# Kernel tuning notes

Measured on AMD Instinct MI355X. Metric: run time of the kernel, lower is better.

Reference implementation:

```python
import jax, jax.numpy as jnp
import numpy as np

B, T, D = 4, 2048, 1024
N_HEADS = 16
D_HEAD = D // N_HEADS


def setup_inputs() -> dict:
    key = jax.random.key(0)
    ks = jax.random.split(key, 5)
    s = 1.0 / np.sqrt(D)  # keep activations well-scaled
    return {
        "x": jax.random.normal(ks[0], (B, T, D), dtype=jnp.float32),
        "Wq": jax.random.normal(ks[1], (D, D), dtype=jnp.float32) * s,
        "Wk": jax.random.normal(ks[2], (D, D), dtype=jnp.float32) * s,
        "Wv": jax.random.normal(ks[3], (D, D), dtype=jnp.float32) * s,
        "Wo": jax.random.normal(ks[4], (D, D), dtype=jnp.float32) * s,
    }


def reference(x, Wq, Wk, Wv, Wo):
    Bx, Tx, C = x.shape
    # projections; nn.Linear(d,d,bias=False): y = x @ W^T
    def split_heads(y):
        return y.reshape(Bx, Tx, N_HEADS, D_HEAD).transpose(0, 2, 1, 3)  # [B,H,T,dh]
    q = split_heads(x @ Wq.T)
    k = split_heads(x @ Wk.T)
    v = split_heads(x @ Wv.T)
    scale = 1.0 / np.sqrt(D_HEAD)
    att = jnp.einsum("bhtd,bhsd->bhts", q, k) * scale  # [B,H,T,T]
    causal = jnp.tril(jnp.ones((Tx, Tx), dtype=bool))
    att = jnp.where(causal[None, None], att, -jnp.inf)
    att = jax.nn.softmax(att, axis=-1)
    y = jnp.einsum("bhts,bhsd->bhtd", att, v)  # [B,H,T,dh]
    y = y.transpose(0, 2, 1, 3).reshape(Bx, Tx, C)
    return y @ Wo.T
```

## Files before the change

### kernel.cpp

```cpp
#include <hip/hip_runtime.h>
#include <cstdint>
#include <cstddef>

typedef unsigned short u16;
typedef short bf16x8 __attribute__((ext_vector_type(8)));
typedef unsigned short u16x8 __attribute__((ext_vector_type(8)));
typedef float f32x4 __attribute__((ext_vector_type(4)));
typedef float f32x16 __attribute__((ext_vector_type(16)));
typedef unsigned u32x2 __attribute__((ext_vector_type(2)));

__device__ __forceinline__ u16 f2bf(float x) {
    union { float f; unsigned int u; } v; v.f = x;
    unsigned int u = v.u;
    unsigned int r = (u + 0x7fffu + ((u >> 16) & 1u)) >> 16;
    return (u16)r;
}

__device__ __forceinline__ unsigned cvtpk(float lo, float hi) {
    unsigned r;
    asm("v_cvt_pk_bf16_f32 %0, %1, %2" : "=v"(r) : "v"(lo), "v"(hi));
    return r;
}

__device__ __forceinline__ float exp2v(float x) {
    float y;
    asm("v_exp_f32 %0, %1" : "=v"(y) : "v"(x));
    return y;
}

__device__ __forceinline__ void load_lds16(const void* g, void* l) {
    __builtin_amdgcn_global_load_lds((const __attribute__((address_space(1))) void*)g,
                                     (__attribute__((address_space(3))) void*)l, 16, 0, 0);
}

__global__ void cast_f32_bf16(const float* __restrict__ in, u16* __restrict__ out, int n) {
    int i = (blockIdx.x * blockDim.x + threadIdx.x) * 4;
    int stride = gridDim.x * blockDim.x * 4;
    for (; i < n; i += stride) {
        float4 f = *reinterpret_cast<const float4*>(in + i);
        ushort4 o;
        o.x = f2bf(f.x); o.y = f2bf(f.y); o.z = f2bf(f.z); o.w = f2bf(f.w);
        *reinterpret_cast<ushort4*>(out + i) = o;
    }
}

__global__ void cast_w4(const float* __restrict__ w0, const float* __restrict__ w1,
                        const float* __restrict__ w2, const float* __restrict__ w3,
                        u16* __restrict__ out, int nw) {
    const int wsel = blockIdx.y;
    const float* in = (wsel == 0) ? w0 : (wsel == 1) ? w1 : (wsel == 2) ? w2 : w3;
    u16* o = out + (size_t)wsel * nw;
    int i = (blockIdx.x * blockDim.x + threadIdx.x) * 4;
    int stride = gridDim.x * blockDim.x * 4;
    for (; i < nw; i += stride) {
        float4 f = *reinterpret_cast<const float4*>(in + i);
        ushort4 v;
        v.x = f2bf(f.x); v.y = f2bf(f.y); v.z = f2bf(f.z); v.w = f2bf(f.w);
        *reinterpret_cast<ushort4*>(o + i) = v;
    }
}

template <int MODE>
__global__ __launch_bounds__(256) void gemm_bt(const u16* __restrict__ A,
                                               const u16* __restrict__ Bw,
                                               void* __restrict__ outp,
                                               u16* __restrict__ vtg,
                                               int M, int N, int K) {
    __shared__ u16 smem[16384];
    u16* As = smem;
    u16* Bs = smem + 4096;

    const int tid  = threadIdx.x;
    const int m0   = blockIdx.x * 128;
    const int n0   = blockIdx.y * 128;
    const int wid  = tid >> 6;
    const int lane = tid & 63;
    const int wr   = (wid >> 1) * 64;
    const int wc   = (wid & 1) * 64;
    const int fr   = lane & 15;
    const int ko   = (lane >> 4) * 8;
    const int rq   = (lane >> 4) * 4;

    f32x4 acc[4][4];
#pragma unroll
    for (int i = 0; i < 4; ++i)
#pragma unroll
        for (int j = 0; j < 4; ++j) acc[i][j] = f32x4{0.f, 0.f, 0.f, 0.f};

    const int lr4 = lane >> 2;
    const int ls  = lane & 3;

    for (int k0 = 0; k0 < K; k0 += 32) {
#pragma unroll
        for (int t = 0; t < 2; ++t) {
            const int qtr = wid * 2 + t;
            const int r   = qtr * 16 + lr4;
            load_lds16(&A[(size_t)(m0 + r) * K + k0 + ls * 8], &As[qtr * 512]);
            load_lds16(&Bw[(size_t)(n0 + r) * K + k0 + ls * 8], &Bs[qtr * 512]);
        }
        __syncthreads();

        bf16x8 af[4], bfr[4];
#pragma unroll
        for (int mf = 0; mf < 4; ++mf)
            af[mf] = *reinterpret_cast<const bf16x8*>(&As[(wr + mf * 16 + fr) * 32 + ko]);
#pragma unroll
        for (int nf = 0; nf < 4; ++nf)
            bfr[nf] = *reinterpret_cast<const bf16x8*>(&Bs[(wc + nf * 16 + fr) * 32 + ko]);
        __builtin_amdgcn_s_setprio(1);
#pragma unroll
        for (int mf = 0; mf < 4; ++mf)
#pragma unroll
            for (int nf = 0; nf < 4; ++nf)
                acc[mf][nf] = __builtin_amdgcn_mfma_f32_16x16x32_bf16(
                    af[mf], bfr[nf], acc[mf][nf], 0, 0, 0);
        __builtin_amdgcn_s_setprio(0);
        __syncthreads();
    }

    if constexpr (MODE == 0) {
        float* C = (float*)outp;
#pragma unroll
        for (int mf = 0; mf < 4; ++mf)
#pragma unroll
            for (int nf = 0; nf < 4; ++nf)
#pragma unroll
                for (int i = 0; i < 4; ++i)
                    C[(size_t)(m0 + wr + mf * 16 + rq + i) * N + n0 + wc + nf * 16 + fr] =
                        acc[mf][nf][i];
    } else {
        if (n0 < 2048) {
            const float osc = (n0 < 1024) ? 0.18033688011112042f : 1.0f;
            u16* qk = (u16*)outp;
#pragma unroll
            for (int mf = 0; mf < 4; ++mf)
#pragma unroll
                for (int nf = 0; nf < 4; ++nf)
#pragma unroll
                    for (int i = 0; i < 4; ++i)
                        qk[(size_t)(m0 + wr + mf * 16 + rq + i) * 2048 + n0 + wc + nf * 16 + fr] =
                            f2bf(acc[mf][nf][i] * osc);
        } else {
#pragma unroll
            for (int mf = 0; mf < 4; ++mf)
#pragma unroll
                for (int nf = 0; nf < 4; ++nf) {
                    const int nl  = wc + nf * 16 + fr;
                    const int ml0 = wr + mf * 16 + rq;
                    uint2 pk;
                    pk.x = cvtpk(acc[mf][nf][0], acc[mf][nf][1]);
                    pk.y = cvtpk(acc[mf][nf][2], acc[mf][nf][3]);
                    *reinterpret_cast<uint2*>(
                        &smem[nl * 128 + ((((ml0 * 2) ^ ((nl & 15) << 4))) >> 1)]) = pk;
                }
            __syncthreads();
            const int bb   = m0 >> 11;
            const int tloc = m0 & 2047;
#pragma unroll
            for (int p = 0; p < 8; ++p) {
                const int nl = (tid >> 4) + p * 16;
                const int sl = tid & 15;
                u16x8 v = *reinterpret_cast<const u16x8*>(
                    &smem[nl * 128 + ((((sl * 16) ^ ((nl & 15) << 4))) >> 1)]);
                *reinterpret_cast<u16x8*>(
                    &vtg[(size_t)(bb * 1024 + (n0 - 2048) + nl) * 2048 + tloc + sl * 8]) = v;
            }
        }
    }
}

__global__ __launch_bounds__(128) void attn_fwd(const u16* __restrict__ qk,
                                                const u16* __restrict__ vtg,
                                                u16* __restrict__ Y) {
    constexpr int T = 2048, DQK = 2048, DOUT = 1024;
    const int bh = blockIdx.x;
    const int jb = blockIdx.y;
    const int b  = bh >> 4, hd = bh & 15;
    const int tid = threadIdx.x, w = tid >> 6, lane = tid & 63;
    const int qloc = lane & 31, h2 = lane >> 5;

    __shared__ u16 Ks[2][4096];
    __shared__ u16 Vs[2][4096];

    const size_t rowb = (size_t)b * T;
    const int sr8 = lane >> 3, ss = lane & 7;
    const int sc = (ss ^ sr8) * 8;

#define BUILD_PA(sv, RB, dst) {                                               \
        unsigned wa  = cvtpk(sv[RB + 0], sv[RB + 1]);                         \
        unsigned wb  = cvtpk(sv[RB + 2], sv[RB + 3]);                         \
        unsigned wc2 = cvtpk(sv[RB + 4], sv[RB + 5]);                         \
        unsigned wd  = cvtpk(sv[RB + 6], sv[RB + 7]);                         \
        u32x2 r0 = __builtin_amdgcn_permlane32_swap(wa, wc2, false, false);   \
        u32x2 r1 = __builtin_amdgcn_permlane32_swap(wb, wd, false, false);    \
        dst.x = r0.x; dst.y = r1.x; dst.z = r0.y; dst.w = r1.y; }

#define PV_STEP(pa, KS, ROWBASE, oacc) {                                      \
        const int rr_ = (ROWBASE) + qloc;                                     \
        bf16x8 vf_ = *reinterpret_cast<const bf16x8*>(                        \
            &Vb[rr_ * 64 + (((2 * (KS) + h2) ^ (rr_ & 7)) * 8)]);             \
        oacc = __builtin_amdgcn_mfma_f32_32x32x16_bf16(                       \
            *reinterpret_cast<const bf16x8*>(&pa), vf_, oacc, 0, 0, 0); }

    for (int qi = 0; qi < 2; ++qi) {
        const int qt = (qi == 0) ? (31 - jb) : jb;
        const int q0 = qt * 64;
        const int wq = q0 + w * 32;
        const int NT = qt + 1;

        bf16x8 qf[4];
#pragma unroll
        for (int ks = 0; ks < 4; ++ks)
            qf[ks] = *reinterpret_cast<const bf16x8*>(
                &qk[(rowb + wq + qloc) * DQK + hd * 64 + ks * 16 + h2 * 8]);

        f32x16 o0, o1;
#pragma unroll
        for (int i = 0; i < 16; ++i) { o0[i] = 0.f; o1[i] = 0.f; }
        float lp = 0.f;

        const u16* kp[4];
        const u16* vp[4];
#pragma unroll
        for (int t = 0; t < 4; ++t) {
            const int r = (w * 4 + t) * 8 + sr8;
            kp[t] = qk + (rowb + r) * DQK + 1024 + hd * 64 + sc;
            vp[t] = vtg + ((size_t)bh * 64 + r) * T + sc;
        }

        __syncthreads();

#pragma unroll
        for (int t = 0; t < 4; ++t) {
            const int chunk = w * 4 + t;
            load_lds16(kp[t], &Ks[0][chunk * 512]);
            load_lds16(vp[t], &Vs[0][chunk * 512]);
        }
#pragma unroll
        for (int t = 0; t < 4; ++t) { kp[t] += 64 * DQK; vp[t] += 64; }

        for (int kt = 0; kt < NT; ++kt) {
            __syncthreads();

            if (kt + 1 < NT) {
                const int nb = (kt + 1) & 1;
#pragma unroll
                for (int t = 0; t < 4; ++t) {
                    const int chunk = w * 4 + t;
                    load_lds16(kp[t], &Ks[nb][chunk * 512]);
                    load_lds16(vp[t], &Vs[nb][chunk * 512]);
                }
#pragma unroll
                for (int t = 0; t < 4; ++t) { kp[t] += 64 * DQK; vp[t] += 64; }
            }

            const int k0 = kt * 64;
            if (k0 <= wq + 31) {
                const u16* Kb = Ks[kt & 1];
                const u16* Vb = Vs[kt & 1];
                const bool do1 = (k0 + 32 <= wq + 31);
                const bool dm  = (k0 + 63 > wq);

                f32x16 st0, st1;
#pragma unroll
                for (int i = 0; i < 16; ++i) { st0[i] = 0.f; st1[i] = 0.f; }

                __builtin_amdgcn_s_setprio(1);
#pragma unroll
                for (int ks = 0; ks < 4; ++ks) {
                    bf16x8 kf = *reinterpret_cast<const bf16x8*>(
                        &Kb[qloc * 64 + (((2 * ks + h2) ^ (qloc & 7)) * 8)]);
                    st0 = __builtin_amdgcn_mfma_f32_32x32x16_bf16(kf, qf[ks], st0, 0, 0, 0);
                }
                if (do1) {
#pragma unroll
                    for (int ks = 0; ks < 4; ++ks) {
                        const int r1 = 32 + qloc;
                        bf16x8 kf = *reinterpret_cast<const bf16x8*>(
                            &Kb[r1 * 64 + (((2 * ks + h2) ^ (r1 & 7)) * 8)]);
                        st1 = __builtin_amdgcn_mfma_f32_32x32x16_bf16(kf, qf[ks], st1, 0, 0, 0);
                    }
                }
                __builtin_amdgcn_s_setprio(0);

                const int qg = wq + qloc;
#pragma unroll
                for (int i = 0; i < 16; ++i) st0[i] = exp2v(st0[i]);
                if (do1) {
#pragma unroll
                    for (int i = 0; i < 16; ++i) st1[i] = exp2v(st1[i]);
                }
                if (dm) {
#pragma unroll
                    for (int r = 0; r < 16; ++r) {
                        const int crow = (r & 3) + 8 * (r >> 2) + 4 * h2;
                        if (k0 + crow > qg)      st0[r] = 0.f;
                        if (k0 + 32 + crow > qg) st1[r] = 0.f;
                    }
                }
                {
                    float l0 = 0.f, l1 = 0.f, l2 = 0.f, l3 = 0.f;
#pragma unroll
                    for (int i = 0; i < 4; ++i) {
                        l0 += st0[i]; l1 += st0[4 + i]; l2 += st0[8 + i]; l3 += st0[12 + i];
                    }
                    if (do1) {
#pragma unroll
                        for (int i = 0; i < 4; ++i) {
                            l0 += st1[i]; l1 += st1[4 + i]; l2 += st1[8 + i]; l3 += st1[12 + i];
                        }
                    }
                    lp += (l0 + l1) + (l2 + l3);
                }

                uint4 pa0, pa1, pa2, pa3;
                BUILD_PA(st0, 0, pa0);
                BUILD_PA(st0, 8, pa1);
                if (do1) {
                    BUILD_PA(st1, 0, pa2);
                    BUILD_PA(st1, 8, pa3);
                }

                __builtin_amdgcn_s_setprio(1);
                PV_STEP(pa0, 0, 0, o0);
                PV_STEP(pa1, 1, 0, o0);
                PV_STEP(pa0, 0, 32, o1);
                PV_STEP(pa1, 1, 32, o1);
                if (do1) {
                    PV_STEP(pa2, 2, 0, o0);
                    PV_STEP(pa3, 3, 0, o0);
                    PV_STEP(pa2, 2, 32, o1);
                    PV_STEP(pa3, 3, 32, o1);
                }
                __builtin_amdgcn_s_setprio(0);
            }
        }

        const float lf = lp + __shfl_xor(lp, 32);
        const float linv = 1.0f / lf;
#pragma unroll
        for (int r = 0; r < 16; ++r) {
            const int crow = (r & 3) + 8 * (r >> 2) + 4 * h2;
            const float rl = __shfl(linv, crow);
            const size_t yrow = rowb + wq + crow;
            Y[yrow * DOUT + hd * 64 + qloc]      = (u16)cvtpk(o0[r] * rl, 0.f);
            Y[yrow * DOUT + hd * 64 + 32 + qloc] = (u16)cvtpk(o1[r] * rl, 0.f);
        }
    }
#undef BUILD_PA
#undef PV_STEP
}

extern "C" void kernel_launch(void* const* d_in, const int* in_sizes, int n_in,
                              void* d_out, int out_size, void* d_ws, size_t ws_size,
                              hipStream_t stream) {
    const float* x  = (const float*)d_in[0];
    const float* Wq = (const float*)d_in[1];
    const float* Wk = (const float*)d_in[2];
    const float* Wv = (const float*)d_in[3];
    const float* Wo = (const float*)d_in[4];

    constexpr int B = 4, T = 2048, D = 1024;
    constexpr int M = B * T;
    const int nx = in_sizes[0];
    const int nw = in_sizes[1];

    char* ws = (char*)d_ws;
    u16* xb   = (u16*)(ws);
    u16* qkb  = (u16*)(ws + (16ull << 20));
    u16* vtg  = (u16*)(ws + (48ull << 20));
    u16* yb   = (u16*)(ws + (64ull << 20));
    u16* wqkv = (u16*)(ws + (80ull << 20));
    u16* wob  = wqkv + 3 * (size_t)nw;

    cast_f32_bf16<<<2048, 256, 0, stream>>>(x, xb, nx);
    cast_w4<<<dim3(256, 4), 256, 0, stream>>>(Wq, Wk, Wv, Wo, wqkv, nw);

    gemm_bt<1><<<dim3(M / 128, 3072 / 128), 256, 0, stream>>>(xb, wqkv, qkb, vtg, M, 3072, D);

    attn_fwd<<<dim3(64, 16), 128, 0, stream>>>(qkb, vtg, yb);

    gemm_bt<0><<<dim3(M / 128, D / 128), 256, 0, stream>>>(yb, wob, d_out, nullptr, M, D, D);
}
```

Before: 179.2 us.

## Add dedicated 256x256 QKV GEMM with triple-buffered async LDS loads

Replaces the templated 128x128 QKV projection GEMM with a dedicated 512-thread kernel using 256x256 tiles, a three-stage LDS ring filled by direct global-to-LDS loads with explicit vmcnt waits, and swizzled LDS layouts. The epilogue stages the Q/K outputs through LDS so they are written as coalesced 16-byte rows, and V is transposed in two halves. The goal is more reuse per loaded tile and overlap of loads with MFMA work in the largest GEMM. In exchange it uses 96KB of LDS and many accumulator registers per thread, which can lower occupancy, and it gives fewer blocks (384) to spread over the CUs.

```diff
diff --git a/kernel.cpp b/kernel.cpp
--- a/kernel.cpp
+++ b/kernel.cpp
@@ -60,12 +60,166 @@
     }
 }
 
-template <int MODE>
-__global__ __launch_bounds__(256) void gemm_bt(const u16* __restrict__ A,
-                                               const u16* __restrict__ Bw,
-                                               void* __restrict__ outp,
-                                               u16* __restrict__ vtg,
-                                               int M, int N, int K) {
+__global__ __launch_bounds__(512, 2) void gemm_qkv(const u16* __restrict__ A,
+                                                   const u16* __restrict__ Bw,
+                                                   u16* __restrict__ qkout,
+                                                   u16* __restrict__ vtg) {
+    constexpr int K = 1024, NT = 32;
+    __shared__ u16 smem[49152];
+
+    const int tid  = threadIdx.x;
+    const int m0   = blockIdx.x * 256;
+    const int n0   = blockIdx.y * 256;
+    const int wid  = tid >> 6, lane = tid & 63;
+    const int fr   = lane & 15, g = lane >> 4;
+    const int wm   = wid >> 2, wn = wid & 3;
+
+    const int r0   = tid >> 2;
+    const int ssrc = (tid & 3) ^ ((r0 >> 1) & 3);
+    const int wb   = (tid & ~63) * 8;
+    const u16* pA0 = A  + (size_t)(m0 + r0) * K + ssrc * 8;
+    const u16* pA1 = A  + (size_t)(m0 + r0 + 128) * K + ssrc * 8;
+    const u16* pB0 = Bw + (size_t)(n0 + r0) * K + ssrc * 8;
+    const u16* pB1 = Bw + (size_t)(n0 + r0 + 128) * K + ssrc * 8;
+
+    int offA[8], offB[4];
+#pragma unroll
+    for (int mf = 0; mf < 8; ++mf) {
+        const int row = wm * 128 + mf * 16 + fr;
+        offA[mf] = row * 32 + (g ^ ((row >> 1) & 3)) * 8;
+    }
+#pragma unroll
+    for (int nfr = 0; nfr < 4; ++nfr) {
+        const int row = wn * 64 + nfr * 16 + fr;
+        offB[nfr] = 8192 + row * 32 + (g ^ ((row >> 1) & 3)) * 8;
+    }
+
+    f32x4 acc[8][4];
+#pragma unroll
+    for (int i = 0; i < 8; ++i)
+#pragma unroll
+        for (int j = 0; j < 4; ++j) acc[i][j] = f32x4{0.f, 0.f, 0.f, 0.f};
+
+#define ISSUE(BUF) {                                                   \
+        load_lds16(pA0, &smem[(BUF) * 16384 + wb]);                    \
+        load_lds16(pA1, &smem[(BUF) * 16384 + 4096 + wb]);             \
+        load_lds16(pB0, &smem[(BUF) * 16384 + 8192 + wb]);             \
+        load_lds16(pB1, &smem[(BUF) * 16384 + 12288 + wb]);            \
+        pA0 += 32; pA1 += 32; pB0 += 32; pB1 += 32; }
+
+    ISSUE(0);
+    ISSUE(1);
+
+    int b = 0;
+    for (int t = 0; t < NT; ++t) {
+        if (t < NT - 1) asm volatile("s_waitcnt vmcnt(4)\n\ts_barrier" ::: "memory");
+        else            asm volatile("s_waitcnt vmcnt(0)\n\ts_barrier" ::: "memory");
+
+        if (t + 2 < NT) {
+            const int b2 = (b == 0) ? 2 : b - 1;
+            ISSUE(b2);
+        }
+
+        const u16* Tb = &smem[b * 16384];
+        bf16x8 a[8], bv[4];
+#pragma unroll
+        for (int mf = 0; mf < 8; ++mf)
+            a[mf] = *reinterpret_cast<const bf16x8*>(&Tb[offA[mf]]);
+#pragma unroll
+        for (int nfr = 0; nfr < 4; ++nfr)
+            bv[nfr] = *reinterpret_cast<const bf16x8*>(&Tb[offB[nfr]]);
+
+        __builtin_amdgcn_s_setprio(1);
+#pragma unroll
+        for (int mf = 0; mf < 8; ++mf)
+#pragma unroll
+            for (int nfr = 0; nfr < 4; ++nfr)
+                acc[mf][nfr] = __builtin_amdgcn_mfma_f32_16x16x32_bf16(
+                    a[mf], bv[nfr], acc[mf][nfr], 0, 0, 0);
+        __builtin_amdgcn_s_setprio(0);
+
+        b = (b == 2) ? 0 : b + 1;
+    }
+#undef ISSUE
+
+    __syncthreads();
+
+    char* sb = reinterpret_cast<char*>(smem);
+    if (n0 < 2048) {
+        const float osc = (n0 < 1024) ? 0.18033688011112042f : 1.0f;
+#pragma unroll
+        for (int half = 0; half < 2; ++half) {
+            if (wm == half) {
+#pragma unroll
+                for (int mf = 0; mf < 8; ++mf)
+#pragma unroll
+                    for (int nfr = 0; nfr < 4; ++nfr) {
+                        const int rl  = mf * 16 + g * 4;
+                        const int col = wn * 64 + nfr * 16 + fr;
+#pragma unroll
+                        for (int i = 0; i < 4; ++i) {
+                            const int row  = rl + i;
+                            const int byte = row * 512 + ((col * 2) ^ (((row >> 2) & 3) << 5));
+                            *reinterpret_cast<u16*>(sb + byte) = f2bf(acc[mf][nfr][i] * osc);
+                        }
+                    }
+            }
+            __syncthreads();
+            {
+                const int row = tid >> 2;
+                const int swz = ((row >> 2) & 3) << 5;
+#pragma unroll
+                for (int p = 0; p < 8; ++p) {
+                    const int sl   = (tid & 3) + p * 4;
+                    const int byte = row * 512 + ((sl * 16) ^ swz);
+                    u16x8 v = *reinterpret_cast<const u16x8*>(sb + byte);
+                    *reinterpret_cast<u16x8*>(
+                        &qkout[(size_t)(m0 + half * 128 + row) * 2048 + n0 + sl * 8]) = v;
+                }
+            }
+            __syncthreads();
+        }
+    } else {
+        const int bb = m0 >> 11, tloc = m0 & 2047;
+#pragma unroll
+        for (int half = 0; half < 2; ++half) {
+            if ((wn >> 1) == half) {
+#pragma unroll
+                for (int mf = 0; mf < 8; ++mf)
+#pragma unroll
+                    for (int nfr = 0; nfr < 4; ++nfr) {
+                        const int nl  = (wn & 1) * 64 + nfr * 16 + fr;
+                        const int ml0 = wm * 128 + mf * 16 + g * 4;
+                        const int f   = ((nl & 3) << 5) | (((nl >> 2) & 1) << 4);
+                        uint2 pk;
+                        pk.x = cvtpk(acc[mf][nfr][0], acc[mf][nfr][1]);
+                        pk.y = cvtpk(acc[mf][nfr][2], acc[mf][nfr][3]);
+                        *reinterpret_cast<uint2*>(sb + nl * 512 + ((ml0 * 2) ^ f)) = pk;
+                    }
+            }
+            __syncthreads();
+            {
+                const int nl = tid >> 2;
+                const int f  = ((nl & 3) << 5) | (((nl >> 2) & 1) << 4);
+#pragma unroll
+                for (int p = 0; p < 8; ++p) {
+                    const int sl   = (tid & 3) + p * 4;
+                    const int byte = nl * 512 + ((sl * 16) ^ f);
+                    u16x8 v = *reinterpret_cast<const u16x8*>(sb + byte);
+                    *reinterpret_cast<u16x8*>(
+                        &vtg[(size_t)(bb * 1024 + (n0 - 2048) + half * 128 + nl) * 2048 +
+                             tloc + sl * 8]) = v;
+                }
+            }
+            __syncthreads();
+        }
+    }
+}
+
+__global__ __launch_bounds__(256) void gemm_out(const u16* __restrict__ A,
+                                                const u16* __restrict__ Bw,
+                                                float* __restrict__ C,
+                                                int M, int N, int K) {
     __shared__ u16 smem[16384];
     u16* As = smem;
     u16* Bs = smem + 4096;
@@ -118,55 +272,14 @@
         __syncthreads();
     }
 
-    if constexpr (MODE == 0) {
-        float* C = (float*)outp;
-#pragma unroll
-        for (int mf = 0; mf < 4; ++mf)
-#pragma unroll
-            for (int nf = 0; nf < 4; ++nf)
-#pragma unroll
-                for (int i = 0; i < 4; ++i)
-                    C[(size_t)(m0 + wr + mf * 16 + rq + i) * N + n0 + wc + nf * 16 + fr] =
-                        acc[mf][nf][i];
-    } else {
-        if (n0 < 2048) {
-            const float osc = (n0 < 1024) ? 0.18033688011112042f : 1.0f;
-            u16* qk = (u16*)outp;
-#pragma unroll
-            for (int mf = 0; mf < 4; ++mf)
-#pragma unroll
-                for (int nf = 0; nf < 4; ++nf)
-#pragma unroll
-                    for (int i = 0; i < 4; ++i)
-                        qk[(size_t)(m0 + wr + mf * 16 + rq + i) * 2048 + n0 + wc + nf * 16 + fr] =
-                            f2bf(acc[mf][nf][i] * osc);
-        } else {
-#pragma unroll
-            for (int mf = 0; mf < 4; ++mf)
-#pragma unroll
-                for (int nf = 0; nf < 4; ++nf) {
-                    const int nl  = wc + nf * 16 + fr;
-                    const int ml0 = wr + mf * 16 + rq;
-                    uint2 pk;
-                    pk.x = cvtpk(acc[mf][nf][0], acc[mf][nf][1]);
-                    pk.y = cvtpk(acc[mf][nf][2], acc[mf][nf][3]);
-                    *reinterpret_cast<uint2*>(
-                        &smem[nl * 128 + ((((ml0 * 2) ^ ((nl & 15) << 4))) >> 1)]) = pk;
-                }
-            __syncthreads();
-            const int bb   = m0 >> 11;
-            const int tloc = m0 & 2047;
-#pragma unroll
-            for (int p = 0; p < 8; ++p) {
-                const int nl = (tid >> 4) + p * 16;
-                const int sl = tid & 15;
-                u16x8 v = *reinterpret_cast<const u16x8*>(
-                    &smem[nl * 128 + ((((sl * 16) ^ ((nl & 15) << 4))) >> 1)]);
-                *reinterpret_cast<u16x8*>(
-                    &vtg[(size_t)(bb * 1024 + (n0 - 2048) + nl) * 2048 + tloc + sl * 8]) = v;
-            }
-        }
-    }
+#pragma unroll
+    for (int mf = 0; mf < 4; ++mf)
+#pragma unroll
+        for (int nf = 0; nf < 4; ++nf)
+#pragma unroll
+            for (int i = 0; i < 4; ++i)
+                C[(size_t)(m0 + wr + mf * 16 + rq + i) * N + n0 + wc + nf * 16 + fr] =
+                    acc[mf][nf][i];
 }
 
 __global__ __launch_bounds__(128) void attn_fwd(const u16* __restrict__ qk,
@@ -188,11 +301,11 @@
 
 #define BUILD_PA(sv, RB, dst) {                                               \
         unsigned wa  = cvtpk(sv[RB + 0], sv[RB + 1]);                         \
-        unsigned wb  = cvtpk(sv[RB + 2], sv[RB + 3]);                         \
+        unsigned wb2 = cvtpk(sv[RB + 2], sv[RB + 3]);                         \
         unsigned wc2 = cvtpk(sv[RB + 4], sv[RB + 5]);                         \
         unsigned wd  = cvtpk(sv[RB + 6], sv[RB + 7]);                         \
         u32x2 r0 = __builtin_amdgcn_permlane32_swap(wa, wc2, false, false);   \
-        u32x2 r1 = __builtin_amdgcn_permlane32_swap(wb, wd, false, false);    \
+        u32x2 r1 = __builtin_amdgcn_permlane32_swap(wb2, wd, false, false);   \
         dst.x = r0.x; dst.y = r1.x; dst.z = r0.y; dst.w = r1.y; }
 
 #define PV_STEP(pa, KS, ROWBASE, oacc) {                                      \
@@ -376,9 +489,9 @@
     cast_f32_bf16<<<2048, 256, 0, stream>>>(x, xb, nx);
     cast_w4<<<dim3(256, 4), 256, 0, stream>>>(Wq, Wk, Wv, Wo, wqkv, nw);
 
-    gemm_bt<1><<<dim3(M / 128, 3072 / 128), 256, 0, stream>>>(xb, wqkv, qkb, vtg, M, 3072, D);
+    gemm_qkv<<<dim3(M / 256, 3072 / 256), 512, 0, stream>>>(xb, wqkv, qkb, vtg);
 
     attn_fwd<<<dim3(64, 16), 128, 0, stream>>>(qkb, vtg, yb);
 
-    gemm_bt<0><<<dim3(M / 128, D / 128), 256, 0, stream>>>(yb, wob, d_out, nullptr, M, D, D);
-}
+    gemm_out<<<dim3(M / 128, D / 128), 256, 0, stream>>>(yb, wob, (float*)d_out, M, D, D);
+}
```

Result: faster. 169.6 us (-5.3%).
